# Performance work log

Measured on AMD Instinct MI355X. Metric: run time of the kernel, lower is better.

Reference implementation:

```python
import jax, jax.numpy as jnp
import numpy as np

B, T, IN_DIM = 8, 1024, 512
NUM_HEADS, H_DIM = 8, 64
OUT_DIM = NUM_HEADS * H_DIM
MAX_POS = 512


def setup_inputs() -> dict:
    key = jax.random.key(0)
    ks = jax.random.split(key, 9)
    s = 0.02
    return {
        "x": jax.random.normal(ks[0], (B, T, IN_DIM), dtype=jnp.float32),
        "Wq": jax.random.normal(ks[1], (IN_DIM, OUT_DIM), dtype=jnp.float32) * s,
        "bq": jax.random.normal(ks[2], (OUT_DIM,), dtype=jnp.float32) * s,
        "Wkv": jax.random.normal(ks[3], (IN_DIM, 2 * OUT_DIM), dtype=jnp.float32) * s,
        "bkv": jax.random.normal(ks[4], (2 * OUT_DIM,), dtype=jnp.float32) * s,
        "Wout": jax.random.normal(ks[5], (OUT_DIM, IN_DIM), dtype=jnp.float32) * s,
        "bout": jax.random.normal(ks[6], (IN_DIM,), dtype=jnp.float32) * s,
        "rel_emb": jax.random.normal(ks[7], (2 * MAX_POS + 1, H_DIM), dtype=jnp.float32) * s,
    }


def reference(x, Wq, bq, Wkv, bkv, Wout, bout, rel_emb):
    b, t, _ = x.shape
    scale = H_DIM ** -0.5
    q = x @ Wq + bq                      # [b, t, H*D]
    kv = x @ Wkv + bkv                   # [b, t, 2*H*D]
    k, v = jnp.split(kv, 2, axis=-1)

    def split_heads(a):
        return a.reshape(b, t, NUM_HEADS, H_DIM).transpose(0, 2, 1, 3)  # b h t d

    q, k, v = map(split_heads, (q, k, v))
    dots = jnp.einsum("bhnd,bhmd->bhnm", q, k) * scale

    seq = jnp.arange(t)
    dist = jnp.clip(seq[:, None] - seq[None, :], -MAX_POS, MAX_POS) + MAX_POS  # [n, m]
    rel_pos = rel_emb[dist]              # [n, m, d]
    pos_attn = jnp.einsum("bhnd,nmd->bhnm", q, rel_pos) * scale

    attn = jax.nn.softmax(dots + pos_attn, axis=-1)
    out = jnp.einsum("bhnm,bhmd->bhnd", attn, v)
    out = out.transpose(0, 2, 1, 3).reshape(b, t, OUT_DIM)
    return out @ Wout + bout             # dropout p=0 -> identity
```

## Files before the change

kernel.cpp:

```cpp
#include <hip/hip_runtime.h>

#define BB 8
#define TT 1024
#define NH 8
#define HD 64
#define QT 128

typedef unsigned short u16;
typedef __attribute__((ext_vector_type(8))) short bf16x8;
typedef __attribute__((ext_vector_type(16))) float f32x16;

__device__ __forceinline__ float bf2f(u16 s) {
    union { unsigned u; float f; } v; v.u = ((unsigned)s) << 16; return v.f;
}
__device__ __forceinline__ u16 f2bf(float f) {
    union { float f; unsigned u; } v; v.f = f;
    unsigned r = (v.u + 0x7FFFu + ((v.u >> 16) & 1u)) >> 16;
    return (u16)r;
}
__device__ __forceinline__ float bperm(int byte_idx, float v) {
    union { float f; int i; } a; a.f = v;
    union { int i; float f; } b;
    b.i = __builtin_amdgcn_ds_bpermute(byte_idx, a.i);
    return b.f;
}
__device__ __forceinline__ void gload_lds16(const u16* g, u16* l) {
    __builtin_amdgcn_global_load_lds(
        (const __attribute__((address_space(1))) unsigned int*)g,
        (__attribute__((address_space(3))) unsigned int*)l, 16, 0, 0);
}

#define MFMA(a, b, c) __builtin_amdgcn_mfma_f32_32x32x16_bf16((a), (b), (c), 0, 0, 0)

#define NX4 1048576
#define NR4 16400
#define NMISC (NX4 + NR4)
#define CVT_MISC_BLOCKS 1041
__global__ __launch_bounds__(256) void cvt_all(
    const float* __restrict__ x, const float* __restrict__ rel,
    const float* __restrict__ Wq, const float* __restrict__ Wkv,
    const float* __restrict__ Wout,
    u16* __restrict__ xb, u16* __restrict__ relb,
    u16* __restrict__ WqT, u16* __restrict__ WkvT, u16* __restrict__ WoutT)
{
    __shared__ float tile[64][65];
    const int tid = threadIdx.x;

    if (blockIdx.x < CVT_MISC_BLOCKS) {
        size_t base = (size_t)blockIdx.x * 1024 + tid;
#pragma unroll
        for (int it = 0; it < 4; it++) {
            size_t i = base + it * 256;
            if (i >= NMISC) break;
            const float* src; u16* dst;
            if (i < NX4) { src = x; dst = xb; }
            else { i -= NX4; src = rel; dst = relb; }
            float4 f = *(const float4*)(src + i * 4);
            ushort4 o;
            o.x = f2bf(f.x); o.y = f2bf(f.y); o.z = f2bf(f.z); o.w = f2bf(f.w);
            *(ushort4*)(dst + i * 4) = o;
        }
        return;
    }

    int bid = blockIdx.x - CVT_MISC_BLOCKS;
    const float* W; u16* Wt; int N, kt, ct;
    if (bid < 64)       { W = Wq;   Wt = WqT;   N = 512;  kt = (bid >> 3) * 64; ct = (bid & 7) * 64; }
    else if (bid < 192) { bid -= 64;  W = Wkv;  Wt = WkvT; N = 1024; kt = (bid >> 4) * 64; ct = (bid & 15) * 64; }
    else                { bid -= 192; W = Wout; Wt = WoutT; N = 512;  kt = (bid >> 3) * 64; ct = (bid & 7) * 64; }

#pragma unroll
    for (int i = 0; i < 16; i++) {
        int e = tid + i * 256;
        int r = e >> 6, c = e & 63;
        tile[r][c] = W[(size_t)(kt + r) * N + ct + c];
    }
    __syncthreads();
#pragma unroll
    for (int i = 0; i < 16; i++) {
        int e = tid + i * 256;
        int rr = e >> 6, cc = e & 63;
        Wt[(size_t)(ct + rr) * 512 + kt + cc] = f2bf(tile[cc][rr]);
    }
}

#define GEMM_STAGE(As, Bs, Abase, Bbase, k0)                                   \
    {                                                                          \
        const int wb16 = (tid & 192) * 8;   \
        _Pragma("unroll")                                                      \
        for (int i = 0; i < 4; i++) {                                          \
            int slot = i * 256 + tid;                                          \
            int row = slot >> 3;                                               \
            int c16 = (slot & 7) ^ (row & 7);                                  \
            gload_lds16(Abase + (size_t)row * 512 + (k0) + c16 * 8,            \
                        As + i * 2048 + wb16);                                 \
            gload_lds16(Bbase + (size_t)row * 512 + (k0) + c16 * 8,            \
                        Bs + i * 2048 + wb16);                                 \
        }                                                                      \
    }

#define GEMM_COMPUTE(As, Bs, ar_base, br_base)                                 \
    {                                                                          \
        _Pragma("unroll")                                                      \
        for (int ks = 0; ks < 4; ks++) {                                       \
            bf16x8 a0, a1, b0, b1;                                             \
            {                                                                  \
                int r0_ = (ar_base), r1_ = (ar_base) + 32;                     \
                int q0_ = (br_base), q1_ = (br_base) + 32;                     \
                a0 = *(const bf16x8*)(As + r0_ * 64 +                          \
                                      (((2 * ks + lh) ^ (r0_ & 7)) * 8));      \
                a1 = *(const bf16x8*)(As + r1_ * 64 +                          \
                                      (((2 * ks + lh) ^ (r1_ & 7)) * 8));      \
                b0 = *(const bf16x8*)(Bs + q0_ * 64 +                          \
                                      (((2 * ks + lh) ^ (q0_ & 7)) * 8));      \
                b1 = *(const bf16x8*)(Bs + q1_ * 64 +                          \
                                      (((2 * ks + lh) ^ (q1_ & 7)) * 8));      \
            }                                                                  \
            acc[0][0] = MFMA(a0, b0, acc[0][0]);                               \
            acc[0][1] = MFMA(a0, b1, acc[0][1]);                               \
            acc[1][0] = MFMA(a1, b0, acc[1][0]);                               \
            acc[1][1] = MFMA(a1, b1, acc[1][1]);                               \
        }                                                                      \
    }

__global__ __launch_bounds__(256) void gemm_qkv(
    const u16* __restrict__ A, const u16* __restrict__ Bt,
    const float* __restrict__ bq, const float* __restrict__ bkv,
    u16* __restrict__ oq, u16* __restrict__ ok, u16* __restrict__ ov)
{
    __shared__ __align__(16) u16 As[128 * 64];
    __shared__ __align__(16) u16 Bs[128 * 64];

    const int tid = threadIdx.x;
    const int lane = tid & 63, w = tid >> 6;
    const int l31 = lane & 31, lh = lane >> 5;
    const int wr = w & 1, wc = w >> 1;
    const int row0 = blockIdx.x * 128 + 64 * wr;
    const int c0g  = blockIdx.y * 128 + 64 * wc;

    const u16* Abase = A  + (size_t)blockIdx.x * 128 * 512;
    const u16* Bbase = Bt + (size_t)blockIdx.y * 128 * 512;
    const int ar_base = 64 * wr + l31;
    const int br_base = 64 * wc + l31;

    f32x16 acc[2][2];
#pragma unroll
    for (int i = 0; i < 2; i++)
#pragma unroll
        for (int j = 0; j < 2; j++)
#pragma unroll
            for (int e = 0; e < 16; e++) acc[i][j][e] = 0.f;

    for (int kk = 0; kk < 8; kk++) {
        GEMM_STAGE(As, Bs, Abase, Bbase, kk * 64);
        __syncthreads();
        GEMM_COMPUTE(As, Bs, ar_base, br_base);
        __syncthreads();
    }

    const int rbase = 4 * lh;
#pragma unroll
    for (int ri = 0; ri < 2; ri++) {
#pragma unroll
        for (int ci = 0; ci < 2; ci++) {
            const int r0 = row0 + 32 * ri;
            const int gc = c0g + 32 * ci + l31;
            if (gc < 512) {
                const float bv = bq[gc];
                const int h = gc >> 6, d = gc & 63;
#pragma unroll
                for (int rg = 0; rg < 16; rg++) {
                    int gr = r0 + (rg & 3) + 8 * (rg >> 2) + rbase;
                    int b = gr >> 10, t = gr & 1023;
                    oq[(((size_t)b * NH + h) * TT + t) * HD + d] =
                        f2bf((acc[ri][ci][rg] + bv) * 0.18033688f);
                }
            } else if (gc < 1024) {
                const float bv = bkv[gc - 512];
                const int h = (gc - 512) >> 6, d = gc & 63;
#pragma unroll
                for (int rg = 0; rg < 16; rg++) {
                    int gr = r0 + (rg & 3) + 8 * (rg >> 2) + rbase;
                    int b = gr >> 10, t = gr & 1023;
                    ok[(((size_t)b * NH + h) * TT + t) * HD + d] =
                        f2bf(acc[ri][ci][rg] + bv);
                }
            } else {
                const float bv = bkv[gc - 512];
                const int vcol = gc - 1024;
                const int h = vcol >> 6, d = vcol & 63;
                const int b = r0 >> 10;
                const int t0 = (r0 & 1023) + rbase;
                size_t base = (((size_t)b * NH + h) * HD + d) * TT;
#pragma unroll
                for (int g = 0; g < 4; g++) {
                    ushort4 p;
                    p.x = f2bf(acc[ri][ci][4 * g + 0] + bv);
                    p.y = f2bf(acc[ri][ci][4 * g + 1] + bv);
                    p.z = f2bf(acc[ri][ci][4 * g + 2] + bv);
                    p.w = f2bf(acc[ri][ci][4 * g + 3] + bv);
                    *(ushort4*)&ov[base + t0 + 8 * g] = p;
                }
            }
        }
    }
}

__global__ __launch_bounds__(256) void gemm_out(
    const u16* __restrict__ A, const u16* __restrict__ Bt,
    const float* __restrict__ bias, float* __restrict__ of)
{
    __shared__ __align__(16) u16 As[128 * 64];
    __shared__ __align__(16) u16 Bs[64 * 64];

    const int tid = threadIdx.x;
    const int lane = tid & 63, w = tid >> 6;
    const int l31 = lane & 31, lh = lane >> 5;
    const int wr = w & 1, wc = w >> 1;
    const int row0 = blockIdx.x * 128 + 64 * wr;

    const u16* Abase = A  + (size_t)blockIdx.x * 128 * 512;
    const u16* Bbase = Bt + (size_t)blockIdx.y * 64 * 512;
    const int ar_base = 64 * wr + l31;
    const int br_base = 32 * wc + l31;

    f32x16 acc0, acc1;
#pragma unroll
    for (int i = 0; i < 16; i++) { acc0[i] = 0.f; acc1[i] = 0.f; }

    for (int kk = 0; kk < 8; kk++) {
        {
            const int wb16 = (tid & 192) * 8;
#pragma unroll
            for (int i = 0; i < 4; i++) {
                int slot = i * 256 + tid;
                int row = slot >> 3;
                int c16 = (slot & 7) ^ (row & 7);
                gload_lds16(Abase + (size_t)row * 512 + kk * 64 + c16 * 8,
                            As + i * 2048 + wb16);
            }
#pragma unroll
            for (int i = 0; i < 2; i++) {
                int slot = i * 256 + tid;
                int row = slot >> 3;
                int c16 = (slot & 7) ^ (row & 7);
                gload_lds16(Bbase + (size_t)row * 512 + kk * 64 + c16 * 8,
                            Bs + i * 2048 + wb16);
            }
        }
        __syncthreads();
#pragma unroll
        for (int ks = 0; ks < 4; ks++) {
            int r0_ = ar_base, r1_ = ar_base + 32, q0_ = br_base;
            bf16x8 a0 = *(const bf16x8*)(As + r0_ * 64 +
                                         (((2 * ks + lh) ^ (r0_ & 7)) * 8));
            bf16x8 a1 = *(const bf16x8*)(As + r1_ * 64 +
                                         (((2 * ks + lh) ^ (r1_ & 7)) * 8));
            bf16x8 b0 = *(const bf16x8*)(Bs + q0_ * 64 +
                                         (((2 * ks + lh) ^ (q0_ & 7)) * 8));
            acc0 = MFMA(a0, b0, acc0);
            acc1 = MFMA(a1, b0, acc1);
        }
        __syncthreads();
    }

    const int rbase = 4 * lh;
    const int gcol = blockIdx.y * 64 + 32 * wc + l31;
    const float bv = bias[gcol];
#pragma unroll
    for (int rg = 0; rg < 16; rg++) {
        int gr = row0 + (rg & 3) + 8 * (rg >> 2) + rbase;
        of[(size_t)gr * 512 + gcol]        = acc0[rg] + bv;
        of[(size_t)(gr + 32) * 512 + gcol] = acc1[rg] + bv;
    }
}

__global__ __launch_bounds__(256) void attn_mfma(
    const u16* __restrict__ q_ws, const u16* __restrict__ k_ws,
    const u16* __restrict__ v_ws, const u16* __restrict__ relb,
    u16* __restrict__ attn_out)
{
    __shared__ __align__(16) u16 GPs[4][32 * 104];

    const int tid  = threadIdx.x;
    const int lane = tid & 63;
    const int w    = tid >> 6;
    const int l31  = lane & 31;
    const int lh   = lane >> 5;
    const int bh   = blockIdx.x;
    const int n0   = blockIdx.y * QT;

    bf16x8 a_q[4];
    {
        const u16* qp = q_ws + (((size_t)bh * TT) + n0 + 32 * w + l31) * HD + 8 * lh;
#pragma unroll
        for (int ks = 0; ks < 4; ks++)
            a_q[ks] = *(const bf16x8*)(qp + 16 * ks);
    }

    f32x16 O0, O1;
    float li[16];
#pragma unroll
    for (int i = 0; i < 16; i++) { O0[i] = 0.f; O1[i] = 0.f; li[i] = 0.f; }

    u16* Gw = GPs[w];
    const int rbase = 4 * lh;
    const u16* kbase = k_ws + (size_t)bh * TT * HD;
    const u16* vbase = v_ws + (size_t)bh * HD * TT;
    const int pbb = n0 + 449 + 32 * w;

    f32x16 zvec;
#pragma unroll
    for (int i = 0; i < 16; i++) zvec[i] = 0.f;
    int bidx16[16];
    int pa0[16], pa1[16];
#pragma unroll
    for (int rg = 0; rg < 16; rg++) {
        int r = (rg & 3) + 8 * (rg >> 2) + rbase;
        bidx16[rg] = (((lh << 5) | ((r - l31 + 31) & 31))) << 2;
        pa0[rg] = r * 104 + (((l31 >> 3) ^ (r & 7)) * 8) + (l31 & 7);
        pa1[rg] = r * 104 + ((((l31 + 32) >> 3) ^ (r & 7)) * 8) + (l31 & 7);
    }
    int pv_off[4];
#pragma unroll
    for (int ms = 0; ms < 4; ms++) {
        int mg = 2 * ms + lh;
        pv_off[ms] = l31 * 104 + ((mg ^ (l31 & 7)) * 8);
    }

    const int kdoff = 8 * lh;

    bf16x8 kf[8], rf[12];
    {
        const u16* k0 = kbase + (size_t)l31 * HD + kdoff;
        const u16* k1 = kbase + (size_t)(l31 + 32) * HD + kdoff;
#pragma unroll
        for (int ks = 0; ks < 4; ks++) {
            kf[2 * ks]     = *(const bf16x8*)(k0 + 16 * ks);
            kf[2 * ks + 1] = *(const bf16x8*)(k1 + 16 * ks);
        }
    }
    f32x16 S0 = MFMA(a_q[0], kf[0], zvec);
    f32x16 S1 = MFMA(a_q[0], kf[1], zvec);
#pragma unroll
    for (int ks = 1; ks < 4; ks++) {
        S0 = MFMA(a_q[ks], kf[2 * ks], S0);
        S1 = MFMA(a_q[ks], kf[2 * ks + 1], S1);
    }
    {
#pragma unroll
        for (int gt = 0; gt < 3; gt++) {
            int p = pbb + 32 * gt + l31;
            p = p < 0 ? 0 : (p > 1024 ? 1024 : p);
            const u16* rb = relb + (size_t)p * HD;
#pragma unroll
            for (int ks = 0; ks < 4; ks++)
                rf[4 * gt + ks] = *(const bf16x8*)(rb + 16 * ks + 8 * lh);
        }
    }
    const u16* kp0 = kbase + (size_t)(64 + l31) * HD + kdoff;
    const u16* kp1 = kbase + (size_t)(64 + l31 + 32) * HD + kdoff;
#pragma unroll
    for (int ks = 0; ks < 4; ks++) {
        kf[2 * ks]     = *(const bf16x8*)(kp0 + 16 * ks);
        kf[2 * ks + 1] = *(const bf16x8*)(kp1 + 16 * ks);
    }
    kp0 += 64 * HD;
    kp1 += 64 * HD;

    const u16* vp0 = vbase + (size_t)l31 * TT + 8 * lh;
    const u16* vp1 = vbase + (size_t)(l31 + 32) * TT + 8 * lh;

    for (int mt = 0; mt < 16; mt++) {

        f32x16 gA = MFMA(a_q[0], rf[0], zvec);
        f32x16 gB = MFMA(a_q[0], rf[4], zvec);
        f32x16 gC = MFMA(a_q[0], rf[8], zvec);
#pragma unroll
        for (int ks = 1; ks < 4; ks++) {
            gA = MFMA(a_q[ks], rf[ks], gA);
            gB = MFMA(a_q[ks], rf[4 + ks], gB);
            gC = MFMA(a_q[ks], rf[8 + ks], gC);
        }

        bf16x8 vf[8];
#pragma unroll
        for (int ms = 0; ms < 4; ms++) {
            const int moff = (2 * ms) * 8;
            vf[2 * ms]     = *(const bf16x8*)(vp0 + moff);
            vf[2 * ms + 1] = *(const bf16x8*)(vp1 + moff);
        }
        vp0 += 64;
        vp1 += 64;

        rf[8]  = rf[0];
        rf[9]  = rf[1];
        rf[10] = rf[2];
        rf[11] = rf[3];
        {
            const int m0n = (mt < 15) ? (mt + 1) * 64 : 0;
            const int pb = pbb - m0n;
            int p0 = pb + l31;       p0 = p0 < 0 ? 0 : (p0 > 1024 ? 1024 : p0);
            int p1 = pb + 32 + l31;  p1 = p1 < 0 ? 0 : (p1 > 1024 ? 1024 : p1);
            const u16* rb0 = relb + (size_t)p0 * HD;
            const u16* rb1 = relb + (size_t)p1 * HD;
#pragma unroll
            for (int ks = 0; ks < 4; ks++) {
                rf[ks]     = *(const bf16x8*)(rb0 + 16 * ks + 8 * lh);
                rf[4 + ks] = *(const bf16x8*)(rb1 + 16 * ks + 8 * lh);
            }
        }

#pragma unroll
        for (int rg = 0; rg < 16; rg++) {
            int r = (rg & 3) + 8 * (rg >> 2) + rbase;
            float mS0 = (l31 >= r) ? gB[rg] : gC[rg];
            float mS1 = (l31 >= r) ? gA[rg] : gB[rg];
            S0[rg] += bperm(bidx16[rg], mS0);
            S1[rg] += bperm(bidx16[rg], mS1);
        }

#pragma unroll
        for (int rg = 0; rg < 16; rg++) {
            float e0, e1;
            asm("v_exp_f32 %0, %1" : "=v"(e0) : "v"(S0[rg]));
            asm("v_exp_f32 %0, %1" : "=v"(e1) : "v"(S1[rg]));
            li[rg] += e0 + e1;
            unsigned pk;
            asm("v_cvt_pk_bf16_f32 %0, %1, %2" : "=v"(pk) : "v"(e0), "v"(e1));
            Gw[pa0[rg]] = (u16)pk;
            Gw[pa1[rg]] = (u16)(pk >> 16);
        }

        if (mt < 15) {
            __builtin_amdgcn_s_setprio(1);
            S0 = MFMA(a_q[0], kf[0], zvec);
            S1 = MFMA(a_q[0], kf[1], zvec);
#pragma unroll
            for (int ks = 1; ks < 4; ks++) {
                S0 = MFMA(a_q[ks], kf[2 * ks], S0);
                S1 = MFMA(a_q[ks], kf[2 * ks + 1], S1);
            }
            __builtin_amdgcn_s_setprio(0);
#pragma unroll
            for (int ks = 0; ks < 4; ks++) {
                kf[2 * ks]     = *(const bf16x8*)(kp0 + 16 * ks);
                kf[2 * ks + 1] = *(const bf16x8*)(kp1 + 16 * ks);
            }
            kp0 = (mt < 13) ? kp0 + 64 * HD : kbase + (size_t)l31 * HD + kdoff;
            kp1 = (mt < 13) ? kp1 + 64 * HD
                            : kbase + (size_t)(l31 + 32) * HD + kdoff;
        }

        __builtin_amdgcn_s_setprio(1);
#pragma unroll
        for (int ms = 0; ms < 4; ms++) {
            bf16x8 a_p = *(const bf16x8*)&Gw[pv_off[ms]];
            O0 = MFMA(a_p, vf[2 * ms], O0);
            O1 = MFMA(a_p, vf[2 * ms + 1], O1);
        }
        __builtin_amdgcn_s_setprio(0);
    }

#pragma unroll
    for (int rg = 0; rg < 16; rg++) {
        float rs = li[rg];
        rs += __shfl_xor(rs, 1);
        rs += __shfl_xor(rs, 2);
        rs += __shfl_xor(rs, 4);
        rs += __shfl_xor(rs, 8);
        rs += __shfl_xor(rs, 16);
        li[rg] = 1.0f / rs;
    }

    const int b = bh >> 3, h = bh & 7;
    u16* ob = attn_out + ((size_t)b * TT + n0 + 32 * w) * 512 + h * 64;
#pragma unroll
    for (int rg = 0; rg < 16; rg++) {
        int r = (rg & 3) + 8 * (rg >> 2) + rbase;
        ob[(size_t)r * 512 + l31]      = f2bf(O0[rg] * li[rg]);
        ob[(size_t)r * 512 + l31 + 32] = f2bf(O1[rg] * li[rg]);
    }
}

extern "C" void kernel_launch(void* const* d_in, const int* in_sizes, int n_in,
                              void* d_out, int out_size, void* d_ws, size_t ws_size,
                              hipStream_t stream)
{
    const float* x    = (const float*)d_in[0];
    const float* Wq   = (const float*)d_in[1];
    const float* bq   = (const float*)d_in[2];
    const float* Wkv  = (const float*)d_in[3];
    const float* bkv  = (const float*)d_in[4];
    const float* Wout = (const float*)d_in[5];
    const float* bout = (const float*)d_in[6];
    const float* rel  = (const float*)d_in[7];
    float* out = (float*)d_out;

    char* ws = (char*)d_ws;
    const size_t MB = 1024 * 1024;
    u16*   q_wsb  = (u16*)(ws);
    u16*   k_wsb  = (u16*)(ws + 8 * MB);
    u16*   v_wsb  = (u16*)(ws + 16 * MB);
    u16*   x_bf   = (u16*)(ws + 24 * MB);
    u16*   a_wsb  = (u16*)(ws + 32 * MB);
    u16*   relb   = (u16*)(ws + 40 * MB);
    u16*   WT_all = (u16*)(ws + 41 * MB);
    u16*   WoutT  = (u16*)(ws + 42 * MB + 512 * 1024);

    cvt_all<<<CVT_MISC_BLOCKS + 256, 256, 0, stream>>>(
        x, rel, Wq, Wkv, Wout, x_bf, relb,
        WT_all, WT_all + 512 * 512, WoutT);

    gemm_qkv<<<dim3(64, 12), 256, 0, stream>>>(
        x_bf, WT_all, bq, bkv, q_wsb, k_wsb, v_wsb);

    attn_mfma<<<dim3(64, 8), 256, 0, stream>>>(
        q_wsb, k_wsb, v_wsb, relb, a_wsb);

    gemm_out<<<dim3(64, 8), 256, 0, stream>>>(a_wsb, WoutT, bout, out);
}
```

Baseline: 210.7 us.

## Double-buffer LDS tiles in QKV and output projection GEMMs

Both projection GEMMs now split each 64-wide K step into two 32-wide steps and keep two LDS buffers. The global-to-LDS load for the next K step is issued before the MFMAs on the current buffer, leaving one barrier per iteration instead of two. The aim is to hide global load latency behind compute, at the cost of twice as many loop iterations and a different XOR swizzle over 4 column groups.

After: 210.5 us. About the same (-0.1%).

```diff
diff --git a/kernel.cpp b/kernel.cpp
--- a/kernel.cpp
+++ b/kernel.cpp
@@ -84,38 +84,35 @@
     }
 }
 
-#define GEMM_STAGE(As, Bs, Abase, Bbase, k0)                                   \
+#define QKV_STAGE(buf, k0)                                                     \
     {                                                                          \
         const int wb16 = (tid & 192) * 8;   \
         _Pragma("unroll")                                                      \
-        for (int i = 0; i < 4; i++) {                                          \
+        for (int i = 0; i < 2; i++) {                                          \
             int slot = i * 256 + tid;                                          \
-            int row = slot >> 3;                                               \
-            int c16 = (slot & 7) ^ (row & 7);                                  \
-            gload_lds16(Abase + (size_t)row * 512 + (k0) + c16 * 8,            \
-                        As + i * 2048 + wb16);                                 \
-            gload_lds16(Bbase + (size_t)row * 512 + (k0) + c16 * 8,            \
-                        Bs + i * 2048 + wb16);                                 \
+            int row = slot >> 2;                                               \
+            int c4 = (slot & 3) ^ (row & 3);                                   \
+            gload_lds16(Abase + (size_t)row * 512 + (k0) + c4 * 8,             \
+                        As[buf] + i * 2048 + wb16);                            \
+            gload_lds16(Bbase + (size_t)row * 512 + (k0) + c4 * 8,             \
+                        Bs[buf] + i * 2048 + wb16);                            \
         }                                                                      \
     }
 
-#define GEMM_COMPUTE(As, Bs, ar_base, br_base)                                 \
+#define QKV_COMPUTE(buf)                                                       \
     {                                                                          \
         _Pragma("unroll")                                                      \
-        for (int ks = 0; ks < 4; ks++) {                                       \
-            bf16x8 a0, a1, b0, b1;                                             \
-            {                                                                  \
-                int r0_ = (ar_base), r1_ = (ar_base) + 32;                     \
-                int q0_ = (br_base), q1_ = (br_base) + 32;                     \
-                a0 = *(const bf16x8*)(As + r0_ * 64 +                          \
-                                      (((2 * ks + lh) ^ (r0_ & 7)) * 8));      \
-                a1 = *(const bf16x8*)(As + r1_ * 64 +                          \
-                                      (((2 * ks + lh) ^ (r1_ & 7)) * 8));      \
-                b0 = *(const bf16x8*)(Bs + q0_ * 64 +                          \
-                                      (((2 * ks + lh) ^ (q0_ & 7)) * 8));      \
-                b1 = *(const bf16x8*)(Bs + q1_ * 64 +                          \
-                                      (((2 * ks + lh) ^ (q1_ & 7)) * 8));      \
-            }                                                                  \
+        for (int ks = 0; ks < 2; ks++) {                                       \
+            const int r0_ = ar_base, r1_ = ar_base + 32;                       \
+            const int q0_ = br_base, q1_ = br_base + 32;                       \
+            bf16x8 a0 = *(const bf16x8*)(As[buf] + r0_ * 32 +                  \
+                                         (((2 * ks + lh) ^ (r0_ & 3)) * 8));   \
+            bf16x8 a1 = *(const bf16x8*)(As[buf] + r1_ * 32 +                  \
+                                         (((2 * ks + lh) ^ (r1_ & 3)) * 8));   \
+            bf16x8 b0 = *(const bf16x8*)(Bs[buf] + q0_ * 32 +                  \
+                                         (((2 * ks + lh) ^ (q0_ & 3)) * 8));   \
+            bf16x8 b1 = *(const bf16x8*)(Bs[buf] + q1_ * 32 +                  \
+                                         (((2 * ks + lh) ^ (q1_ & 3)) * 8));   \
             acc[0][0] = MFMA(a0, b0, acc[0][0]);                               \
             acc[0][1] = MFMA(a0, b1, acc[0][1]);                               \
             acc[1][0] = MFMA(a1, b0, acc[1][0]);                               \
@@ -128,8 +125,8 @@
     const float* __restrict__ bq, const float* __restrict__ bkv,
     u16* __restrict__ oq, u16* __restrict__ ok, u16* __restrict__ ov)
 {
-    __shared__ __align__(16) u16 As[128 * 64];
-    __shared__ __align__(16) u16 Bs[128 * 64];
+    __shared__ __align__(16) u16 As[2][128 * 32];
+    __shared__ __align__(16) u16 Bs[2][128 * 32];
 
     const int tid = threadIdx.x;
     const int lane = tid & 63, w = tid >> 6;
@@ -151,10 +148,12 @@
 #pragma unroll
             for (int e = 0; e < 16; e++) acc[i][j][e] = 0.f;
 
-    for (int kk = 0; kk < 8; kk++) {
-        GEMM_STAGE(As, Bs, Abase, Bbase, kk * 64);
-        __syncthreads();
-        GEMM_COMPUTE(As, Bs, ar_base, br_base);
+    QKV_STAGE(0, 0);
+    __syncthreads();
+    for (int kk = 0; kk < 16; kk++) {
+        const int cur = kk & 1;
+        if (kk < 15) QKV_STAGE(cur ^ 1, (kk + 1) * 32);
+        QKV_COMPUTE(cur);
         __syncthreads();
     }
 
@@ -210,8 +209,8 @@
     const u16* __restrict__ A, const u16* __restrict__ Bt,
     const float* __restrict__ bias, float* __restrict__ of)
 {
-    __shared__ __align__(16) u16 As[128 * 64];
-    __shared__ __align__(16) u16 Bs[64 * 64];
+    __shared__ __align__(16) u16 As[2][128 * 32];
+    __shared__ __align__(16) u16 Bs[2][64 * 32];
 
     const int tid = threadIdx.x;
     const int lane = tid & 63, w = tid >> 6;
@@ -228,36 +227,40 @@
 #pragma unroll
     for (int i = 0; i < 16; i++) { acc0[i] = 0.f; acc1[i] = 0.f; }
 
-    for (int kk = 0; kk < 8; kk++) {
-        {
-            const int wb16 = (tid & 192) * 8;
-#pragma unroll
-            for (int i = 0; i < 4; i++) {
-                int slot = i * 256 + tid;
-                int row = slot >> 3;
-                int c16 = (slot & 7) ^ (row & 7);
-                gload_lds16(Abase + (size_t)row * 512 + kk * 64 + c16 * 8,
-                            As + i * 2048 + wb16);
-            }
-#pragma unroll
-            for (int i = 0; i < 2; i++) {
-                int slot = i * 256 + tid;
-                int row = slot >> 3;
-                int c16 = (slot & 7) ^ (row & 7);
-                gload_lds16(Bbase + (size_t)row * 512 + kk * 64 + c16 * 8,
-                            Bs + i * 2048 + wb16);
-            }
-        }
-        __syncthreads();
-#pragma unroll
-        for (int ks = 0; ks < 4; ks++) {
-            int r0_ = ar_base, r1_ = ar_base + 32, q0_ = br_base;
-            bf16x8 a0 = *(const bf16x8*)(As + r0_ * 64 +
-                                         (((2 * ks + lh) ^ (r0_ & 7)) * 8));
-            bf16x8 a1 = *(const bf16x8*)(As + r1_ * 64 +
-                                         (((2 * ks + lh) ^ (r1_ & 7)) * 8));
-            bf16x8 b0 = *(const bf16x8*)(Bs + q0_ * 64 +
-                                         (((2 * ks + lh) ^ (q0_ & 7)) * 8));
+#define OUT_STAGE(buf, k0)                                                     \
+    {                                                                          \
+        const int wb16 = (tid & 192) * 8;                                      \
+        _Pragma("unroll")                                                      \
+        for (int i = 0; i < 2; i++) {                                          \
+            int slot = i * 256 + tid;                                          \
+            int row = slot >> 2;                                               \
+            int c4 = (slot & 3) ^ (row & 3);                                   \
+            gload_lds16(Abase + (size_t)row * 512 + (k0) + c4 * 8,             \
+                        As[buf] + i * 2048 + wb16);                            \
+        }                                                                      \
+        {                                                                      \
+            int slot = tid;                                                    \
+            int row = slot >> 2;                                               \
+            int c4 = (slot & 3) ^ (row & 3);                                   \
+            gload_lds16(Bbase + (size_t)row * 512 + (k0) + c4 * 8,             \
+                        Bs[buf] + wb16);                                       \
+        }                                                                      \
+    }
+
+    OUT_STAGE(0, 0);
+    __syncthreads();
+    for (int kk = 0; kk < 16; kk++) {
+        const int cur = kk & 1;
+        if (kk < 15) OUT_STAGE(cur ^ 1, (kk + 1) * 32);
+#pragma unroll
+        for (int ks = 0; ks < 2; ks++) {
+            const int r0_ = ar_base, r1_ = ar_base + 32, q0_ = br_base;
+            bf16x8 a0 = *(const bf16x8*)(As[cur] + r0_ * 32 +
+                                         (((2 * ks + lh) ^ (r0_ & 3)) * 8));
+            bf16x8 a1 = *(const bf16x8*)(As[cur] + r1_ * 32 +
+                                         (((2 * ks + lh) ^ (r1_ & 3)) * 8));
+            bf16x8 b0 = *(const bf16x8*)(Bs[cur] + q0_ * 32 +
+                                         (((2 * ks + lh) ^ (q0_ & 3)) * 8));
             acc0 = MFMA(a0, b0, acc0);
             acc1 = MFMA(a1, b0, acc1);
         }
```
